# Kernel optimization log

Measured on AMD Instinct MI355X. Metric: run time of the kernel, lower is better.

The kernel has to match this reference:

```python
import jax, jax.numpy as jnp
import numpy as np

THRESHOLD = 0.5
NEG_POS_RATIO = 3


def cxcy_to_xy(c):
    return jnp.concatenate([c[..., :2] - c[..., 2:] / 2.0, c[..., :2] + c[..., 2:] / 2.0], axis=-1)


def xy_to_cxcy(b):
    return jnp.concatenate([(b[..., :2] + b[..., 2:]) / 2.0, b[..., 2:] - b[..., :2]], axis=-1)


def cxcy_to_gcxgcy(c, p):
    # standard SSD encoding with variances (0.1, 0.2)
    return jnp.concatenate([
        (c[..., :2] - p[..., :2]) / (p[..., 2:] / 10.0),
        jnp.log(c[..., 2:] / p[..., 2:]) * 5.0,
    ], axis=-1)


def jaccard(a, b):
    # a: [n,4] xy boxes, b: [m,4] xy boxes -> [n,m] IoU
    lo = jnp.maximum(a[:, None, :2], b[None, :, :2])
    hi = jnp.minimum(a[:, None, 2:], b[None, :, 2:])
    wh = jnp.clip(hi - lo, 0.0)
    inter = wh[..., 0] * wh[..., 1]
    area_a = (a[:, 2] - a[:, 0]) * (a[:, 3] - a[:, 1])
    area_b = (b[:, 2] - b[:, 0]) * (b[:, 3] - b[:, 1])
    return inter / (area_a[:, None] + area_b[None, :] - inter)


def match_one(boxes_i, labels_i, priors_xy, priors_cxcy):
    # boxes_i: [O,4], labels_i: [O] -> true_locs [P,4], true_classes [P]
    n_obj = boxes_i.shape[0]
    ov = jaccard(boxes_i, priors_xy)                 # [O, P]
    ov_per_prior = ov.max(axis=0)                    # [P]
    obj_idx = jnp.argmax(ov, axis=0)                 # [P]
    prior_per_obj = jnp.argmax(ov, axis=1)           # [O]
    # force each object to own its best prior (scatter overwrite)
    obj_idx = obj_idx.at[prior_per_obj].set(jnp.arange(n_obj))
    ov_per_prior = ov_per_prior.at[prior_per_obj].set(1.0)
    lab = labels_i[obj_idx]                          # [P]
    lab = jnp.where(ov_per_prior < THRESHOLD, 0, lab)
    true_locs = cxcy_to_gcxgcy(xy_to_cxcy(boxes_i[obj_idx]), priors_cxcy)
    return true_locs, lab


def setup_inputs() -> dict:
    key = jax.random.key(0)
    ks = jax.random.split(key, 7)
    B, P, C, O = 64, 8732, 81, 32
    predicted_locs = jax.random.normal(ks[0], (B, P, 4), jnp.float32)
    predicted_scores = jax.random.normal(ks[1], (B, P, C), jnp.float32)
    ctr = jax.random.uniform(ks[2], (B, O, 2), jnp.float32, 0.2, 0.8)
    wh = jax.random.uniform(ks[3], (B, O, 2), jnp.float32, 0.05, 0.3)
    boxes = jnp.concatenate([ctr - wh / 2.0, ctr + wh / 2.0], axis=-1)  # valid xy boxes
    labels = jax.random.randint(ks[4], (B, O), 1, C)                    # nonzero object classes
    pctr = jax.random.uniform(ks[5], (P, 2), jnp.float32, 0.05, 0.95)
    pwh = jax.random.uniform(ks[6], (P, 2), jnp.float32, 0.05, 0.5)
    priors_cxcy = jnp.concatenate([pctr, pwh], axis=-1)
    return {
        'predicted_locs': predicted_locs,
        'predicted_scores': predicted_scores,
        'boxes': boxes,
        'labels': labels,
        'priors_cxcy': priors_cxcy,
    }


def reference(predicted_locs, predicted_scores, boxes, labels, priors_cxcy):
    priors_xy = cxcy_to_xy(priors_cxcy)
    true_locs, true_classes = jax.vmap(match_one, in_axes=(0, 0, None, None))(
        boxes, labels, priors_xy, priors_cxcy)       # [B,P,4], [B,P]

    log_probs = jax.nn.log_softmax(predicted_scores, axis=2)   # [B,P,C]
    bg_loss = -log_probs[:, :, 0]                               # mining score (detached in torch)

    pos_mask = true_classes > 0                                 # [B,P]
    num_pos = pos_mask.sum(axis=1, keepdims=True)               # [B,1]
    num_neg = NEG_POS_RATIO * num_pos
    mined = jnp.where(pos_mask, -jnp.inf, bg_loss)
    idx = jnp.argsort(-mined, axis=1)
    order = jnp.argsort(idx, axis=1)                            # rank of each prior by hardness
    neg_mask = order < num_neg
    mask = pos_mask | neg_mask

    # cross-entropy (sum over selected priors)
    ce = -jnp.take_along_axis(log_probs, true_classes[..., None], axis=2)[..., 0]  # [B,P]
    classification_loss = jnp.sum(ce * mask)

    # smooth-L1 (beta=1, sum over positive priors)
    diff = jnp.abs(predicted_locs - true_locs)
    sl1 = jnp.where(diff < 1.0, 0.5 * diff * diff, diff - 0.5)  # [B,P,4]
    smooth_l1_loss = jnp.sum(sl1.sum(axis=-1) * pos_mask)

    n = num_pos.sum().astype(predicted_locs.dtype)
    return classification_loss / n, smooth_l1_loss / n
```

## Files before the change

kernel.cpp:

```cpp
#include <hip/hip_runtime.h>
#include <stdint.h>

#define NB 64
#define NP 8732
#define NO 32
#define NC 81
#define NTOT (NB*NP)
#define THRESH 0.5f
#define NSEG 8
#define SEGP 1092
#define CLS_BLOCKS 2048
#define NGRP (NTOT/4)
#define KPT 18

typedef unsigned long long ull;
typedef unsigned int uint;

__global__ __launch_bounds__(256)
void k_match1(const float4* __restrict__ boxes4, const float4* __restrict__ priors4,
              unsigned char* __restrict__ pp_g, ull* __restrict__ bkey_part)
{
#pragma clang fp contract(off)
    const int b    = blockIdx.x >> 3;
    const int seg  = blockIdx.x & 7;
    const int tid  = threadIdx.x;
    const int lane = tid & 63, wv = tid >> 6;
    const int p0 = seg * SEGP;
    const int p1 = (p0 + SEGP < NP) ? (p0 + SEGP) : NP;

    __shared__ float bx[NO][4];
    __shared__ float barea[NO];
    __shared__ ull   red[NO][4];

    if (tid < NO) {
        float4 bb = boxes4[b*NO + tid];
        bx[tid][0]=bb.x; bx[tid][1]=bb.y; bx[tid][2]=bb.z; bx[tid][3]=bb.w;
        barea[tid] = (bb.z-bb.x)*(bb.w-bb.y);
    }
    __syncthreads();

    ull bkey[NO];
#pragma unroll
    for (int o = 0; o < NO; ++o) bkey[o] = 0ull;

    for (int p = p0 + tid; p < p1; p += 256) {
        float4 pr = priors4[p];
        float px1 = pr.x - pr.z*0.5f, py1 = pr.y - pr.w*0.5f;
        float px2 = pr.x + pr.z*0.5f, py2 = pr.y + pr.w*0.5f;
        float parea = (px2-px1)*(py2-py1);
        float bestv = -1.0f; int besto = 0;
#pragma unroll
        for (int o = 0; o < NO; ++o) {
            float lx = fmaxf(bx[o][0], px1), ly = fmaxf(bx[o][1], py1);
            float hx = fminf(bx[o][2], px2), hy = fminf(bx[o][3], py2);
            float w = fmaxf(hx - lx, 0.0f), h = fmaxf(hy - ly, 0.0f);
            float inter = w*h;
            float iou = inter / ((barea[o] + parea) - inter);
            if (iou > bestv) { bestv = iou; besto = o; }
            ull key = ((ull)__float_as_uint(iou) << 32) | (uint)(~p);
            if (key > bkey[o]) bkey[o] = key;
        }
        pp_g[(size_t)b*NP + p] =
            (unsigned char)(besto | ((bestv < THRESH) ? 0 : 0x80));
    }

#pragma unroll
    for (int o = 0; o < NO; ++o) {
        ull k = bkey[o];
        for (int off = 32; off > 0; off >>= 1) {
            ull t = __shfl_down(k, (unsigned)off);
            if (t > k) k = t;
        }
        if (lane == 0) red[o][wv] = k;
    }
    __syncthreads();
    if (tid < NO) {
        ull k = red[tid][0];
#pragma unroll
        for (int w = 1; w < 4; ++w) if (red[tid][w] > k) k = red[tid][w];
        bkey_part[(b*NO + tid)*NSEG + seg] = k;
    }
}

__global__ __launch_bounds__(256)
void k_match2(const float4* __restrict__ boxes4, const int* __restrict__ labels,
              const float4* __restrict__ priors4, const float4* __restrict__ plocs4,
              const ull* __restrict__ bkey_part, unsigned char* __restrict__ pp_g,
              int* __restrict__ numpos, float* __restrict__ sl1_part)
{
#pragma clang fp contract(off)
    const int b = blockIdx.x, tid = threadIdx.x;
    const int lane = tid & 63, wv = tid >> 6;

    __shared__ uint  pp_u[NP/4];
    __shared__ float bx[NO][4];
    __shared__ int   ppo[NO];
    __shared__ float redf[4];
    __shared__ int   redi[4];
    unsigned char* pp_s = (unsigned char*)pp_u;

    const uint* src = (const uint*)(pp_g + (size_t)b*NP);
    for (int i = tid; i < NP/4; i += 256) pp_u[i] = src[i];

    if (tid < NO) {
        float4 bb = boxes4[b*NO + tid];
        bx[tid][0]=bb.x; bx[tid][1]=bb.y; bx[tid][2]=bb.z; bx[tid][3]=bb.w;
        const ull* bp = bkey_part + (b*NO + tid)*NSEG;
        ull k = bp[0];
#pragma unroll
        for (int s = 1; s < NSEG; ++s) if (bp[s] > k) k = bp[s];
        ppo[tid] = (int)(~(uint)(k & 0xFFFFFFFFull));
    }
    __syncthreads();

    if (tid < NO) {
        int p = ppo[tid];
        bool win = true;
        for (int o2 = tid + 1; o2 < NO; ++o2) if (ppo[o2] == p) { win = false; break; }
        if (win) {
            unsigned char v = (unsigned char)(tid | 0x80);
            pp_s[p] = v;
            pp_g[(size_t)b*NP + p] = v;
        }
    }
    __syncthreads();

    int cnt = 0; float sl1 = 0.0f;
    for (int p = tid; p < NP; p += 256) {
        int ppv = pp_s[p];
        if (ppv & 0x80) {
            cnt++;
            int oi = ppv & 31;
            float x1 = bx[oi][0], y1 = bx[oi][1], x2 = bx[oi][2], y2 = bx[oi][3];
            float bcx = (x1+x2)*0.5f, bcy = (y1+y2)*0.5f;
            float bw = x2-x1, bh = y2-y1;
            float4 pr = priors4[p];
            float g0 = (bcx - pr.x) / (pr.z / 10.0f);
            float g1 = (bcy - pr.y) / (pr.w / 10.0f);
            float g2 = logf(bw / pr.z) * 5.0f;
            float g3 = logf(bh / pr.w) * 5.0f;
            float4 pl = plocs4[(size_t)b*NP + p];
            float d0 = fabsf(pl.x-g0), d1 = fabsf(pl.y-g1);
            float d2 = fabsf(pl.z-g2), d3 = fabsf(pl.w-g3);
            sl1 += (d0 < 1.f ? 0.5f*d0*d0 : d0-0.5f);
            sl1 += (d1 < 1.f ? 0.5f*d1*d1 : d1-0.5f);
            sl1 += (d2 < 1.f ? 0.5f*d2*d2 : d2-0.5f);
            sl1 += (d3 < 1.f ? 0.5f*d3*d3 : d3-0.5f);
        }
    }
    for (int off = 32; off > 0; off >>= 1) {
        cnt += __shfl_down(cnt, (unsigned)off);
        sl1 += __shfl_down(sl1, (unsigned)off);
    }
    if (lane == 0) { redi[wv] = cnt; redf[wv] = sl1; }
    __syncthreads();
    if (tid == 0) {
        numpos[b]   = redi[0]+redi[1]+redi[2]+redi[3];
        sl1_part[b] = redf[0]+redf[1]+redf[2]+redf[3];
    }
}

__global__ __launch_bounds__(256)
void k_cls(const float* __restrict__ scores, const unsigned char* __restrict__ pp_g,
           const int* __restrict__ labels, uint* __restrict__ mined,
           float* __restrict__ ce_part)
{
    const int tid = threadIdx.x, lane = tid & 63, wv = tid >> 6;
    const int sub = lane >> 4, sl = lane & 15;
    const int wgid = blockIdx.x*4 + wv;
    float ce_acc = 0.f;

    for (int grp = wgid; grp < NGRP; grp += CLS_BLOCKS*4) {
        const int r = grp*4 + sub;
        const float* s = scores + (size_t)r*NC;
        float v0 = s[sl], v1 = s[16+sl], v2 = s[32+sl], v3 = s[48+sl], v4 = s[64+sl];
        float e = __expf(v0)+__expf(v1)+__expf(v2)+__expf(v3)+__expf(v4);
        if (sl == 0) e += __expf(s[80]);
#pragma unroll
        for (int off = 8; off > 0; off >>= 1) e += __shfl_xor(e, off);
        float lse = __logf(e);

        if (sl == 0) {
            int ppv = pp_g[r];
            uint key = 0u;
            if (ppv & 0x80) {
                int bb = r / NP;
                int lb = labels[bb*NO + (ppv & 31)];
                float sv = scores[(size_t)r*NC + lb];
                ce_acc += lse - sv;
            } else {
                key = __float_as_uint(lse - v0);
            }
            mined[r] = key;
        }
    }

    for (int off = 32; off > 0; off >>= 1) ce_acc += __shfl_down(ce_acc, (unsigned)off);
    __shared__ float redf[4];
    if (lane == 0) redf[wv] = ce_acc;
    __syncthreads();
    if (tid == 0) ce_part[blockIdx.x] = redf[0]+redf[1]+redf[2]+redf[3];
}

__global__ __launch_bounds__(512)
void k_mine(const uint* __restrict__ mined, const int* __restrict__ numpos,
            float* __restrict__ mined_sum)
{
    const int b = blockIdx.x, tid = threadIdx.x;
    const int lane = tid & 63, wv = tid >> 6;
    __shared__ int  redi[8];
    __shared__ int  sh_tot;
    __shared__ float redf[8];

    uint key[KPT];
#pragma unroll
    for (int j = 0; j < KPT; ++j) {
        int i = j*512 + tid;
        key[j] = (i < NP) ? mined[(size_t)b*NP + i] : 0u;
    }
    const int np = numpos[b];
    int k = 3*np;
    const int nneg = NP - np;
    if (k > nneg) k = nneg;
    if (k <= 0) { if (tid == 0) mined_sum[b] = 0.f; return; }

    uint uk = 0u;
    for (int bit = 30; bit >= 0; --bit) {
        uint cand = uk | (1u << bit);
        int c = 0;
#pragma unroll
        for (int j = 0; j < KPT; ++j) c += (key[j] >= cand) ? 1 : 0;
        for (int off = 32; off > 0; off >>= 1) c += __shfl_down(c, (unsigned)off);
        if (lane == 0) redi[wv] = c;
        __syncthreads();
        if (tid == 0) {
            int t = 0;
#pragma unroll
            for (int w = 0; w < 8; ++w) t += redi[w];
            sh_tot = t;
        }
        __syncthreads();
        if (sh_tot >= k) uk = cand;
        __syncthreads();
    }

    int cgt = 0; float sum = 0.f;
#pragma unroll
    for (int j = 0; j < KPT; ++j) {
        uint u = key[j];
        if (u > uk) { cgt++; sum += __uint_as_float(u); }
    }
    for (int off = 32; off > 0; off >>= 1) {
        cgt += __shfl_down(cgt, (unsigned)off);
        sum += __shfl_down(sum, (unsigned)off);
    }
    if (lane == 0) { redi[wv] = cgt; redf[wv] = sum; }
    __syncthreads();
    if (tid == 0) {
        int c = 0; float s = 0.f;
#pragma unroll
        for (int w = 0; w < 8; ++w) { c += redi[w]; s += redf[w]; }
        mined_sum[b] = s + (float)(k - c) * __uint_as_float(uk);
    }
}

__global__ __launch_bounds__(256)
void k_final(const float* __restrict__ ce_part, const float* __restrict__ mined_sum,
             const float* __restrict__ sl1_part, const int* __restrict__ numpos,
             float* __restrict__ out)
{
    const int tid = threadIdx.x, lane = tid & 63, wv = tid >> 6;
    float c = 0.f, s = 0.f; int n = 0;
    for (int i = tid; i < CLS_BLOCKS; i += 256) c += ce_part[i];
    if (tid < NB) { c += mined_sum[tid]; s = sl1_part[tid]; n = numpos[tid]; }
    for (int off = 32; off > 0; off >>= 1) {
        c += __shfl_down(c, (unsigned)off);
        s += __shfl_down(s, (unsigned)off);
        n += __shfl_down(n, (unsigned)off);
    }
    __shared__ float rc[4], rs[4]; __shared__ int rn[4];
    if (lane == 0) { rc[wv] = c; rs[wv] = s; rn[wv] = n; }
    __syncthreads();
    if (tid == 0) {
        float cc = rc[0]+rc[1]+rc[2]+rc[3];
        float ss = rs[0]+rs[1]+rs[2]+rs[3];
        float nn = (float)(rn[0]+rn[1]+rn[2]+rn[3]);
        out[0] = cc / nn;
        out[1] = ss / nn;
    }
}

extern "C" void kernel_launch(void* const* d_in, const int* in_sizes, int n_in,
                              void* d_out, int out_size, void* d_ws, size_t ws_size,
                              hipStream_t stream)
{
    const float4* plocs4  = (const float4*)d_in[0];
    const float*  scores  = (const float*) d_in[1];
    const float4* boxes4  = (const float4*)d_in[2];
    const int*    labels  = (const int*)   d_in[3];
    const float4* priors4 = (const float4*)d_in[4];
    float* out = (float*)d_out;

    uint* w = (uint*)d_ws;
    unsigned char* pp_g   = (unsigned char*)w;
    uint*          mined  = w + NTOT/4;
    ull*           bkeyp  = (ull*)(w + NTOT/4 + NTOT);
    int*           numpos = (int*)(bkeyp + NB*NO*NSEG);
    float*         sl1p   = (float*)(numpos + NB);
    float*         msum   = sl1p + NB;
    float*         cep    = msum + NB;

    k_match1<<<NB*NSEG,    256, 0, stream>>>(boxes4, priors4, pp_g, bkeyp);
    k_match2<<<NB,         256, 0, stream>>>(boxes4, labels, priors4, plocs4,
                                             bkeyp, pp_g, numpos, sl1p);
    k_cls   <<<CLS_BLOCKS, 256, 0, stream>>>(scores, pp_g, labels, mined, cep);
    k_mine  <<<NB,         512, 0, stream>>>(mined, numpos, msum);
    k_final <<<1,          256, 0, stream>>>(cep, msum, sl1p, numpos, out);
}
```

Before: 359.1 us.

## Run matching and log-sum-exp concurrently, fold CE into post pass, fuse final reduce

Merges the IoU matching kernel and the log-softmax scoring pass into one launch, with block ranges split by role, so the bandwidth-heavy score read overlaps the compute-heavy matching. Positive-prior cross-entropy and zeroing of the mined keys move into the per-image post-matching kernel, which reads a stored lse array. The final reduction is folded into the mining kernel through a last-block atomic counter, cutting the launch count from five to three. In exchange it writes and reads an extra lse array per prior, and the per-image post kernel does scattered score gathers with only 64 blocks.

```diff
diff --git a/kernel.cpp b/kernel.cpp
--- a/kernel.cpp
+++ b/kernel.cpp
@@ -9,6 +9,7 @@
 #define THRESH 0.5f
 #define NSEG 8
 #define SEGP 1092
+#define MATCH_BLOCKS (NB*NSEG)
 #define CLS_BLOCKS 2048
 #define NGRP (NTOT/4)
 #define KPT 18
@@ -17,76 +18,104 @@
 typedef unsigned int uint;
 
 __global__ __launch_bounds__(256)
-void k_match1(const float4* __restrict__ boxes4, const float4* __restrict__ priors4,
-              unsigned char* __restrict__ pp_g, ull* __restrict__ bkey_part)
+void k_prod(const float4* __restrict__ boxes4, const float4* __restrict__ priors4,
+            const float* __restrict__ scores,
+            unsigned char* __restrict__ pp_g, ull* __restrict__ bkey_part,
+            uint* __restrict__ mined, float* __restrict__ lse_arr,
+            int* __restrict__ done)
 {
-#pragma clang fp contract(off)
-    const int b    = blockIdx.x >> 3;
-    const int seg  = blockIdx.x & 7;
     const int tid  = threadIdx.x;
     const int lane = tid & 63, wv = tid >> 6;
-    const int p0 = seg * SEGP;
-    const int p1 = (p0 + SEGP < NP) ? (p0 + SEGP) : NP;
-
-    __shared__ float bx[NO][4];
-    __shared__ float barea[NO];
-    __shared__ ull   red[NO][4];
-
-    if (tid < NO) {
-        float4 bb = boxes4[b*NO + tid];
-        bx[tid][0]=bb.x; bx[tid][1]=bb.y; bx[tid][2]=bb.z; bx[tid][3]=bb.w;
-        barea[tid] = (bb.z-bb.x)*(bb.w-bb.y);
-    }
-    __syncthreads();
-
-    ull bkey[NO];
-#pragma unroll
-    for (int o = 0; o < NO; ++o) bkey[o] = 0ull;
-
-    for (int p = p0 + tid; p < p1; p += 256) {
-        float4 pr = priors4[p];
-        float px1 = pr.x - pr.z*0.5f, py1 = pr.y - pr.w*0.5f;
-        float px2 = pr.x + pr.z*0.5f, py2 = pr.y + pr.w*0.5f;
-        float parea = (px2-px1)*(py2-py1);
-        float bestv = -1.0f; int besto = 0;
+
+    if (blockIdx.x < MATCH_BLOCKS) {
+#pragma clang fp contract(off)
+        __shared__ float bx[NO][4];
+        __shared__ float barea[NO];
+        __shared__ ull   red[NO][4];
+
+        const int b   = blockIdx.x >> 3;
+        const int seg = blockIdx.x & 7;
+        const int p0 = seg * SEGP;
+        const int p1 = (p0 + SEGP < NP) ? (p0 + SEGP) : NP;
+
+        if (blockIdx.x == 0 && tid == 0) *done = 0;
+
+        if (tid < NO) {
+            float4 bb = boxes4[b*NO + tid];
+            bx[tid][0]=bb.x; bx[tid][1]=bb.y; bx[tid][2]=bb.z; bx[tid][3]=bb.w;
+            barea[tid] = (bb.z-bb.x)*(bb.w-bb.y);
+        }
+        __syncthreads();
+
+        ull bkey[NO];
+#pragma unroll
+        for (int o = 0; o < NO; ++o) bkey[o] = 0ull;
+
+        for (int p = p0 + tid; p < p1; p += 256) {
+            float4 pr = priors4[p];
+            float px1 = pr.x - pr.z*0.5f, py1 = pr.y - pr.w*0.5f;
+            float px2 = pr.x + pr.z*0.5f, py2 = pr.y + pr.w*0.5f;
+            float parea = (px2-px1)*(py2-py1);
+            float bestv = -1.0f; int besto = 0;
+#pragma unroll
+            for (int o = 0; o < NO; ++o) {
+                float lx = fmaxf(bx[o][0], px1), ly = fmaxf(bx[o][1], py1);
+                float hx = fminf(bx[o][2], px2), hy = fminf(bx[o][3], py2);
+                float w = fmaxf(hx - lx, 0.0f), h = fmaxf(hy - ly, 0.0f);
+                float inter = w*h;
+                float iou = inter / ((barea[o] + parea) - inter);
+                if (iou > bestv) { bestv = iou; besto = o; }
+                ull key = ((ull)__float_as_uint(iou) << 32) | (uint)(~p);
+                if (key > bkey[o]) bkey[o] = key;
+            }
+            pp_g[(size_t)b*NP + p] =
+                (unsigned char)(besto | ((bestv < THRESH) ? 0 : 0x80));
+        }
+
 #pragma unroll
         for (int o = 0; o < NO; ++o) {
-            float lx = fmaxf(bx[o][0], px1), ly = fmaxf(bx[o][1], py1);
-            float hx = fminf(bx[o][2], px2), hy = fminf(bx[o][3], py2);
-            float w = fmaxf(hx - lx, 0.0f), h = fmaxf(hy - ly, 0.0f);
-            float inter = w*h;
-            float iou = inter / ((barea[o] + parea) - inter);
-            if (iou > bestv) { bestv = iou; besto = o; }
-            ull key = ((ull)__float_as_uint(iou) << 32) | (uint)(~p);
-            if (key > bkey[o]) bkey[o] = key;
-        }
-        pp_g[(size_t)b*NP + p] =
-            (unsigned char)(besto | ((bestv < THRESH) ? 0 : 0x80));
-    }
-
-#pragma unroll
-    for (int o = 0; o < NO; ++o) {
-        ull k = bkey[o];
-        for (int off = 32; off > 0; off >>= 1) {
-            ull t = __shfl_down(k, (unsigned)off);
-            if (t > k) k = t;
-        }
-        if (lane == 0) red[o][wv] = k;
-    }
-    __syncthreads();
-    if (tid < NO) {
-        ull k = red[tid][0];
-#pragma unroll
-        for (int w = 1; w < 4; ++w) if (red[tid][w] > k) k = red[tid][w];
-        bkey_part[(b*NO + tid)*NSEG + seg] = k;
+            ull k = bkey[o];
+            for (int off = 32; off > 0; off >>= 1) {
+                ull t = __shfl_down(k, (unsigned)off);
+                if (t > k) k = t;
+            }
+            if (lane == 0) red[o][wv] = k;
+        }
+        __syncthreads();
+        if (tid < NO) {
+            ull k = red[tid][0];
+#pragma unroll
+            for (int w = 1; w < 4; ++w) if (red[tid][w] > k) k = red[tid][w];
+            bkey_part[(b*NO + tid)*NSEG + seg] = k;
+        }
+    } else {
+        const int sub = lane >> 4, sl = lane & 15;
+        const int wgid = (blockIdx.x - MATCH_BLOCKS)*4 + wv;
+
+        for (int grp = wgid; grp < NGRP; grp += CLS_BLOCKS*4) {
+            const int r = grp*4 + sub;
+            const float* s = scores + (size_t)r*NC;
+            float v0 = s[sl], v1 = s[16+sl], v2 = s[32+sl], v3 = s[48+sl], v4 = s[64+sl];
+            float e = __expf(v0)+__expf(v1)+__expf(v2)+__expf(v3)+__expf(v4);
+            if (sl == 0) e += __expf(s[80]);
+#pragma unroll
+            for (int off = 8; off > 0; off >>= 1) e += __shfl_xor(e, off);
+            float lse = __logf(e);
+            if (sl == 0) {
+                mined[r]   = __float_as_uint(lse - v0);
+                lse_arr[r] = lse;
+            }
+        }
     }
 }
 
 __global__ __launch_bounds__(256)
-void k_match2(const float4* __restrict__ boxes4, const int* __restrict__ labels,
-              const float4* __restrict__ priors4, const float4* __restrict__ plocs4,
-              const ull* __restrict__ bkey_part, unsigned char* __restrict__ pp_g,
-              int* __restrict__ numpos, float* __restrict__ sl1_part)
+void k_post(const float4* __restrict__ boxes4, const int* __restrict__ labels,
+            const float4* __restrict__ priors4, const float4* __restrict__ plocs4,
+            const float* __restrict__ scores, const float* __restrict__ lse_arr,
+            const ull* __restrict__ bkey_part, const unsigned char* __restrict__ pp_g,
+            uint* __restrict__ mined, int* __restrict__ numpos,
+            float* __restrict__ sl1_part, float* __restrict__ ce2)
 {
 #pragma clang fp contract(off)
     const int b = blockIdx.x, tid = threadIdx.x;
@@ -95,7 +124,7 @@
     __shared__ uint  pp_u[NP/4];
     __shared__ float bx[NO][4];
     __shared__ int   ppo[NO];
-    __shared__ float redf[4];
+    __shared__ float redf[4], redc[4];
     __shared__ int   redi[4];
     unsigned char* pp_s = (unsigned char*)pp_u;
 
@@ -117,15 +146,11 @@
         int p = ppo[tid];
         bool win = true;
         for (int o2 = tid + 1; o2 < NO; ++o2) if (ppo[o2] == p) { win = false; break; }
-        if (win) {
-            unsigned char v = (unsigned char)(tid | 0x80);
-            pp_s[p] = v;
-            pp_g[(size_t)b*NP + p] = v;
-        }
+        if (win) pp_s[p] = (unsigned char)(tid | 0x80);
     }
     __syncthreads();
 
-    int cnt = 0; float sl1 = 0.0f;
+    int cnt = 0; float sl1 = 0.0f, ce = 0.0f;
     for (int p = tid; p < NP; p += 256) {
         int ppv = pp_s[p];
         if (ppv & 0x80) {
@@ -146,71 +171,37 @@
             sl1 += (d1 < 1.f ? 0.5f*d1*d1 : d1-0.5f);
             sl1 += (d2 < 1.f ? 0.5f*d2*d2 : d2-0.5f);
             sl1 += (d3 < 1.f ? 0.5f*d3*d3 : d3-0.5f);
+            size_t r = (size_t)b*NP + p;
+            int lb = labels[b*NO + oi];
+            ce += lse_arr[r] - scores[r*NC + lb];
+            mined[r] = 0u;
         }
     }
     for (int off = 32; off > 0; off >>= 1) {
         cnt += __shfl_down(cnt, (unsigned)off);
         sl1 += __shfl_down(sl1, (unsigned)off);
-    }
-    if (lane == 0) { redi[wv] = cnt; redf[wv] = sl1; }
+        ce  += __shfl_down(ce,  (unsigned)off);
+    }
+    if (lane == 0) { redi[wv] = cnt; redf[wv] = sl1; redc[wv] = ce; }
     __syncthreads();
     if (tid == 0) {
         numpos[b]   = redi[0]+redi[1]+redi[2]+redi[3];
         sl1_part[b] = redf[0]+redf[1]+redf[2]+redf[3];
+        ce2[b]      = redc[0]+redc[1]+redc[2]+redc[3];
     }
 }
 
-__global__ __launch_bounds__(256)
-void k_cls(const float* __restrict__ scores, const unsigned char* __restrict__ pp_g,
-           const int* __restrict__ labels, uint* __restrict__ mined,
-           float* __restrict__ ce_part)
-{
-    const int tid = threadIdx.x, lane = tid & 63, wv = tid >> 6;
-    const int sub = lane >> 4, sl = lane & 15;
-    const int wgid = blockIdx.x*4 + wv;
-    float ce_acc = 0.f;
-
-    for (int grp = wgid; grp < NGRP; grp += CLS_BLOCKS*4) {
-        const int r = grp*4 + sub;
-        const float* s = scores + (size_t)r*NC;
-        float v0 = s[sl], v1 = s[16+sl], v2 = s[32+sl], v3 = s[48+sl], v4 = s[64+sl];
-        float e = __expf(v0)+__expf(v1)+__expf(v2)+__expf(v3)+__expf(v4);
-        if (sl == 0) e += __expf(s[80]);
-#pragma unroll
-        for (int off = 8; off > 0; off >>= 1) e += __shfl_xor(e, off);
-        float lse = __logf(e);
-
-        if (sl == 0) {
-            int ppv = pp_g[r];
-            uint key = 0u;
-            if (ppv & 0x80) {
-                int bb = r / NP;
-                int lb = labels[bb*NO + (ppv & 31)];
-                float sv = scores[(size_t)r*NC + lb];
-                ce_acc += lse - sv;
-            } else {
-                key = __float_as_uint(lse - v0);
-            }
-            mined[r] = key;
-        }
-    }
-
-    for (int off = 32; off > 0; off >>= 1) ce_acc += __shfl_down(ce_acc, (unsigned)off);
-    __shared__ float redf[4];
-    if (lane == 0) redf[wv] = ce_acc;
-    __syncthreads();
-    if (tid == 0) ce_part[blockIdx.x] = redf[0]+redf[1]+redf[2]+redf[3];
-}
-
 __global__ __launch_bounds__(512)
-void k_mine(const uint* __restrict__ mined, const int* __restrict__ numpos,
-            float* __restrict__ mined_sum)
+void k_mine2(const uint* __restrict__ mined, const int* __restrict__ numpos,
+             const float* __restrict__ ce2, const float* __restrict__ sl1_part,
+             float* __restrict__ msum, int* __restrict__ done,
+             float* __restrict__ out)
 {
     const int b = blockIdx.x, tid = threadIdx.x;
     const int lane = tid & 63, wv = tid >> 6;
-    __shared__ int  redi[8];
-    __shared__ int  sh_tot;
+    __shared__ int   redi[8];
     __shared__ float redf[8];
+    __shared__ int   lastflag;
 
     uint key[KPT];
 #pragma unroll
@@ -222,71 +213,66 @@
     int k = 3*np;
     const int nneg = NP - np;
     if (k > nneg) k = nneg;
-    if (k <= 0) { if (tid == 0) mined_sum[b] = 0.f; return; }
-
-    uint uk = 0u;
-    for (int bit = 30; bit >= 0; --bit) {
-        uint cand = uk | (1u << bit);
-        int c = 0;
-#pragma unroll
-        for (int j = 0; j < KPT; ++j) c += (key[j] >= cand) ? 1 : 0;
-        for (int off = 32; off > 0; off >>= 1) c += __shfl_down(c, (unsigned)off);
-        if (lane == 0) redi[wv] = c;
+
+    float result = 0.f;
+    if (k > 0) {
+        uint uk = 0u;
+        for (int bit = 30; bit >= 0; --bit) {
+            uint cand = uk | (1u << bit);
+            int c = 0;
+#pragma unroll
+            for (int j = 0; j < KPT; ++j) c += (key[j] >= cand) ? 1 : 0;
+            for (int off = 32; off > 0; off >>= 1) c += __shfl_down(c, (unsigned)off);
+            if (lane == 0) redi[wv] = c;
+            __syncthreads();
+            int t = redi[0]+redi[1]+redi[2]+redi[3]+redi[4]+redi[5]+redi[6]+redi[7];
+            if (t >= k) uk = cand;
+            __syncthreads();
+        }
+
+        int cgt = 0; float sum = 0.f;
+#pragma unroll
+        for (int j = 0; j < KPT; ++j) {
+            uint u = key[j];
+            if (u > uk) { cgt++; sum += __uint_as_float(u); }
+        }
+        for (int off = 32; off > 0; off >>= 1) {
+            cgt += __shfl_down(cgt, (unsigned)off);
+            sum += __shfl_down(sum, (unsigned)off);
+        }
+        if (lane == 0) { redi[wv] = cgt; redf[wv] = sum; }
         __syncthreads();
         if (tid == 0) {
-            int t = 0;
-#pragma unroll
-            for (int w = 0; w < 8; ++w) t += redi[w];
-            sh_tot = t;
-        }
-        __syncthreads();
-        if (sh_tot >= k) uk = cand;
-        __syncthreads();
-    }
-
-    int cgt = 0; float sum = 0.f;
-#pragma unroll
-    for (int j = 0; j < KPT; ++j) {
-        uint u = key[j];
-        if (u > uk) { cgt++; sum += __uint_as_float(u); }
-    }
-    for (int off = 32; off > 0; off >>= 1) {
-        cgt += __shfl_down(cgt, (unsigned)off);
-        sum += __shfl_down(sum, (unsigned)off);
-    }
-    if (lane == 0) { redi[wv] = cgt; redf[wv] = sum; }
+            int c = 0; float s = 0.f;
+#pragma unroll
+            for (int w = 0; w < 8; ++w) { c += redi[w]; s += redf[w]; }
+            result = s + (float)(k - c) * __uint_as_float(uk);
+        }
+    }
+
+    if (tid == 0) {
+        atomicExch(&msum[b], result);
+        __threadfence();
+        lastflag = (atomicAdd(done, 1) == NB-1) ? 1 : 0;
+    }
     __syncthreads();
-    if (tid == 0) {
-        int c = 0; float s = 0.f;
-#pragma unroll
-        for (int w = 0; w < 8; ++w) { c += redi[w]; s += redf[w]; }
-        mined_sum[b] = s + (float)(k - c) * __uint_as_float(uk);
-    }
-}
-
-__global__ __launch_bounds__(256)
-void k_final(const float* __restrict__ ce_part, const float* __restrict__ mined_sum,
-             const float* __restrict__ sl1_part, const int* __restrict__ numpos,
-             float* __restrict__ out)
-{
-    const int tid = threadIdx.x, lane = tid & 63, wv = tid >> 6;
-    float c = 0.f, s = 0.f; int n = 0;
-    for (int i = tid; i < CLS_BLOCKS; i += 256) c += ce_part[i];
-    if (tid < NB) { c += mined_sum[tid]; s = sl1_part[tid]; n = numpos[tid]; }
-    for (int off = 32; off > 0; off >>= 1) {
-        c += __shfl_down(c, (unsigned)off);
-        s += __shfl_down(s, (unsigned)off);
-        n += __shfl_down(n, (unsigned)off);
-    }
-    __shared__ float rc[4], rs[4]; __shared__ int rn[4];
-    if (lane == 0) { rc[wv] = c; rs[wv] = s; rn[wv] = n; }
-    __syncthreads();
-    if (tid == 0) {
-        float cc = rc[0]+rc[1]+rc[2]+rc[3];
-        float ss = rs[0]+rs[1]+rs[2]+rs[3];
-        float nn = (float)(rn[0]+rn[1]+rn[2]+rn[3]);
-        out[0] = cc / nn;
-        out[1] = ss / nn;
+    if (lastflag) {
+        __threadfence();
+        float c = 0.f, s = 0.f; int n = 0;
+        if (tid < NB) {
+            c = ce2[tid] + atomicAdd(&msum[tid], 0.0f);
+            s = sl1_part[tid];
+            n = numpos[tid];
+        }
+        for (int off = 32; off > 0; off >>= 1) {
+            c += __shfl_down(c, (unsigned)off);
+            s += __shfl_down(s, (unsigned)off);
+            n += __shfl_down(n, (unsigned)off);
+        }
+        if (tid == 0) {
+            out[0] = c / (float)n;
+            out[1] = s / (float)n;
+        }
     }
 }
 
@@ -302,18 +288,19 @@
     float* out = (float*)d_out;
 
     uint* w = (uint*)d_ws;
-    unsigned char* pp_g   = (unsigned char*)w;
-    uint*          mined  = w + NTOT/4;
-    ull*           bkeyp  = (ull*)(w + NTOT/4 + NTOT);
-    int*           numpos = (int*)(bkeyp + NB*NO*NSEG);
-    float*         sl1p   = (float*)(numpos + NB);
-    float*         msum   = sl1p + NB;
-    float*         cep    = msum + NB;
-
-    k_match1<<<NB*NSEG,    256, 0, stream>>>(boxes4, priors4, pp_g, bkeyp);
-    k_match2<<<NB,         256, 0, stream>>>(boxes4, labels, priors4, plocs4,
-                                             bkeyp, pp_g, numpos, sl1p);
-    k_cls   <<<CLS_BLOCKS, 256, 0, stream>>>(scores, pp_g, labels, mined, cep);
-    k_mine  <<<NB,         512, 0, stream>>>(mined, numpos, msum);
-    k_final <<<1,          256, 0, stream>>>(cep, msum, sl1p, numpos, out);
+    unsigned char* pp_g    = (unsigned char*)w;
+    uint*          mined   = w + NTOT/4;
+    float*         lse_arr = (float*)(w + NTOT/4 + NTOT);
+    ull*           bkeyp   = (ull*)(w + NTOT/4 + NTOT + NTOT);
+    int*           numpos  = (int*)(bkeyp + NB*NO*NSEG);
+    float*         sl1p    = (float*)(numpos + NB);
+    float*         msum    = sl1p + NB;
+    float*         ce2     = msum + NB;
+    int*           done    = (int*)(ce2 + NB);
+
+    k_prod <<<MATCH_BLOCKS+CLS_BLOCKS, 256, 0, stream>>>(boxes4, priors4, scores,
+                                                         pp_g, bkeyp, mined, lse_arr, done);
+    k_post <<<NB, 256, 0, stream>>>(boxes4, labels, priors4, plocs4, scores, lse_arr,
+                                    bkeyp, pp_g, mined, numpos, sl1p, ce2);
+    k_mine2<<<NB, 512, 0, stream>>>(mined, numpos, ce2, sl1p, msum, done, out);
 }
```

New measurement: 433.4 us. +20.7%, slower.
